# Optimization experiments

Hardware: AMD Instinct MI355X
Metric: run time of the kernel (lower is better)

Reference implementation:

```python
import jax, jax.numpy as jnp
import numpy as np

THRESHOLD = 1.0  # CIF firing threshold (init kwarg)


def setup_inputs() -> dict:
    key = jax.random.key(0)
    k1, k2 = jax.random.split(key)
    B, T, H = 32, 2048, 512
    return {
        "hidden": jax.random.normal(k1, (B, T, H), dtype=jnp.float32),
        "alphas": jax.random.uniform(k2, (B, T), dtype=jnp.float32),
        "integrate": jnp.zeros((B,), dtype=jnp.float32),
        "frame": jnp.zeros((B, H), dtype=jnp.float32),
    }


def cif_scan(hidden, alphas, integrate, frame, threshold):
    """Continuous integrate-and-fire recurrence over time, vectorized over batch.

    hidden: [B,T,H], alphas: [B,T], integrate: [B], frame: [B,H]
    Returns fires [B,T], frames [B,T,H], integrate_new [B], frame_new [B,H].
    """

    def step(carry, inp):
        integ, fr = carry          # [B], [B,H]
        alpha, h_t = inp           # [B], [B,H]
        dist_completion = 1.0 - integ
        integ = integ + alpha
        fire = integ >= threshold                       # [B] bool
        integ_next = jnp.where(fire, integ - 1.0, integ)
        cur = jnp.where(fire, dist_completion, alpha)   # weight spent this step
        rem = alpha - cur                               # leftover weight after firing
        fr_out = fr + cur[:, None] * h_t                # frame recorded at this step
        fr_next = jnp.where(fire[:, None], rem[:, None] * h_t, fr_out)
        return (integ_next, fr_next), (integ, fr_out)

    xs = (jnp.swapaxes(alphas, 0, 1), jnp.swapaxes(hidden, 0, 1))  # time-major
    (integ_f, frame_f), (fires_t, frames_t) = jax.lax.scan(step, (integrate, frame), xs)
    fires = jnp.swapaxes(fires_t, 0, 1)    # [B,T]
    frames = jnp.swapaxes(frames_t, 0, 1)  # [B,T,H]
    return fires, frames, integ_f, frame_f


def reference(hidden, alphas, integrate, frame):
    T = hidden.shape[1]
    fires, frames, integ_new, frame_new = cif_scan(hidden, alphas, integrate, frame, THRESHOLD)
    # torch.index_select(frames[0], 0, nonzero(fires[0] >= threshold)) -> data-dependent
    # shape; emulate with jit-safe padded nonzero (padding rows replicate row 0).
    idx = jnp.nonzero(fires[0] >= THRESHOLD, size=T, fill_value=0)[0]
    frame_sel = frames[0][idx]  # [T, H], first num_fires rows are the fired frames
    return frame_sel, integ_new, frame_new
```

## Files before the change

kernel.cpp:

```cpp
#include <hip/hip_runtime.h>


#define THRESH 1.0f
#define MAX_T 2048

__global__ __launch_bounds__(256) void cif_transpose_kernel(
    const float4* __restrict__ a4, float4* __restrict__ aT4, int B, int T4)
{
    int tid = blockIdx.x * blockDim.x + threadIdx.x;
    if (tid >= B * T4) return;
    int b = tid / T4, c = tid - b * T4;
    aT4[(size_t)c * B + b] = a4[tid];
}

__global__ __launch_bounds__(64) void cif_scan_kernel(
    const float4* __restrict__ aT4,
    const float*  __restrict__ integ0,
    float* __restrict__ gT,
    unsigned long long* __restrict__ fireMask,
    int* __restrict__ rowStart, int* __restrict__ rowEnd, int* __restrict__ rowFlags,
    int* __restrict__ tlast,
    float* __restrict__ integ_out,
    int B, int T)
{
    const int lane = threadIdx.x;
    const int nchunk = T >> 6;
    __shared__ int s_fire[MAX_T];
    __shared__ unsigned long long s_mask[64];
    __shared__ int s_nf, s_f0;

    const bool act = lane < B;
    float integ = act ? integ0[lane] : 0.0f;
    int   lastc = -1;
    unsigned long long lastm = 0;

    float4 bufA[16], bufB[16];

#define LOADCH(buf, c) do { if (act) { \
    _Pragma("unroll") for (int j = 0; j < 16; ++j) \
        buf[j] = aT4[(size_t)((c) * 16 + j) * B + lane]; } } while (0)

#define DOCH(buf, c) do { if (act) { \
    unsigned lo = 0, hi = 0; \
    _Pragma("unroll") for (int j = 0; j < 16; ++j) { \
        const float av[4] = {buf[j].x, buf[j].y, buf[j].z, buf[j].w}; \
        _Pragma("unroll") for (int k = 0; k < 4; ++k) { \
            const int idx = j * 4 + k; \
            const float alpha = av[k]; \
            const float s   = integ + alpha;       \
            const bool fire = (s >= THRESH);       \
            const float sm1 = s - 1.0f;            \
            integ = fire ? sm1 : s; \
            const float gv = fire ? sm1 : alpha;   \
            if (idx < 32) lo |= fire ? (1u << idx) : 0u; \
            else          hi |= fire ? (1u << (idx - 32)) : 0u; \
            gT[(size_t)((c) * 64 + idx) * B + lane] = gv; \
        } } \
    const unsigned long long m = ((unsigned long long)hi << 32) | lo; \
    fireMask[(size_t)(c) * B + lane] = m; \
    if (lane == 0) s_mask[(c)] = m; \
    lastc = m ? (c) : lastc; \
    lastm = m ? m : lastm; \
    } } while (0)

    LOADCH(bufA, 0);
    for (int c = 0; c < nchunk; c += 2) {
        if (c + 1 < nchunk) LOADCH(bufB, c + 1);
        DOCH(bufA, c);
        if (c + 2 < nchunk) LOADCH(bufA, c + 2);
        if (c + 1 < nchunk) DOCH(bufB, c + 1);
    }
#undef LOADCH
#undef DOCH

    if (act) {
        integ_out[lane] = integ;
        tlast[lane] = (lastc >= 0) ? (lastc * 64 + 63 - __clzll(lastm)) : -1;
    }
    __syncthreads();

    unsigned long long m0 = (lane < nchunk) ? s_mask[lane] : 0ull;
    int pc = __popcll(m0);
    int x = pc;
#pragma unroll
    for (int d = 1; d < 64; d <<= 1) {
        int y = __shfl_up(x, d);
        if (lane >= d) x += y;
    }
    const int excl = x - pc;
    if (lane == 63) s_nf = x;
    if (lane == 0)  s_f0 = (int)(m0 & 1ull);
    {
        unsigned long long m = m0; int r = excl;
        while (m) {
            int p = __ffsll((unsigned long long)m) - 1;
            s_fire[r++] = lane * 64 + p;
            m &= m - 1;
        }
    }
    __syncthreads();

    const int nf = s_nf, f0 = s_f0;
    for (int r = lane; r < T; r += 64) {
        int st, en, fl;
        if (r < nf) {
            en = s_fire[r];
            st = (r == 0) ? 0 : s_fire[r - 1];
            fl = ((r == 0) ? 1 : 0) | 2;
        } else {
            st = 0; en = 0; fl = 1 | (f0 ? 2 : 0);
        }
        rowStart[r] = st; rowEnd[r] = en; rowFlags[r] = fl;
    }
}

__global__ __launch_bounds__(128) void cif_out_kernel(
    const float* __restrict__ hidden,
    const float* __restrict__ frame0,
    const float* __restrict__ gT,
    const float* __restrict__ alphas,
    const int* __restrict__ rowStart, const int* __restrict__ rowEnd,
    const int* __restrict__ rowFlags, const int* __restrict__ tlast,
    float* __restrict__ out_sel,
    float* __restrict__ frame_out,
    int B, int T, int H)
{
    const int blk = blockIdx.x;

    if (blk < T) {
        const int r = blk;
        const int start = rowStart[r], end = rowEnd[r], fl = rowFlags[r];
        const float a  = alphas[end];
        const float ge = gT[(size_t)end * B];
        const float wend = (fl & 2) ? (a - ge) : a;
        for (int h0 = threadIdx.x * 4; h0 < H; h0 += 128 * 4) {
            float4 acc = (fl & 1) ? *reinterpret_cast<const float4*>(frame0 + h0)
                                  : make_float4(0.f, 0.f, 0.f, 0.f);
            for (int s = start; s < end; ++s) {
                const float  w  = gT[(size_t)s * B];
                const float4 hv = *reinterpret_cast<const float4*>(hidden + (size_t)s * H + h0);
                acc.x += w * hv.x; acc.y += w * hv.y;
                acc.z += w * hv.z; acc.w += w * hv.w;
            }
            const float4 hv = *reinterpret_cast<const float4*>(hidden + (size_t)end * H + h0);
            acc.x += wend * hv.x; acc.y += wend * hv.y;
            acc.z += wend * hv.z; acc.w += wend * hv.w;
            *reinterpret_cast<float4*>(out_sel + (size_t)r * H + h0) = acc;
        }
    } else {
        const int b  = blk - T;
        const int tl = tlast[b];
        const int start = (tl < 0) ? 0 : tl;
        const float* hb = hidden + (size_t)b * T * H;
        for (int h0 = threadIdx.x * 4; h0 < H; h0 += 128 * 4) {
            float4 acc = (tl < 0) ? *reinterpret_cast<const float4*>(frame0 + (size_t)b * H + h0)
                                  : make_float4(0.f, 0.f, 0.f, 0.f);
            for (int s = start; s < T; ++s) {
                const float  w  = gT[(size_t)s * B + b];
                const float4 hv = *reinterpret_cast<const float4*>(hb + (size_t)s * H + h0);
                acc.x += w * hv.x; acc.y += w * hv.y;
                acc.z += w * hv.z; acc.w += w * hv.w;
            }
            *reinterpret_cast<float4*>(frame_out + (size_t)b * H + h0) = acc;
        }
    }
}

extern "C" void kernel_launch(void* const* d_in, const int* in_sizes, int n_in,
                              void* d_out, int out_size, void* d_ws, size_t ws_size,
                              hipStream_t stream) {
    const float* hidden    = (const float*)d_in[0];
    const float* alphas    = (const float*)d_in[1];
    const float* integrate = (const float*)d_in[2];
    const float* frame     = (const float*)d_in[3];

    const int B = in_sizes[2];
    const int T = in_sizes[1] / B;
    const int H = in_sizes[3] / B;

    float* out       = (float*)d_out;
    float* out_sel   = out;
    float* integ_out = out + (size_t)T * H;
    float* frame_out = integ_out + B;

    char* ws = (char*)d_ws;
    float4* aT4 = (float4*)ws;                 ws += sizeof(float) * (size_t)B * T;
    float*  gT  = (float*)ws;                  ws += sizeof(float) * (size_t)B * T;
    unsigned long long* fireMask = (unsigned long long*)ws; ws += sizeof(unsigned long long) * (size_t)(T / 64) * B;
    int* rowStart = (int*)ws;                  ws += sizeof(int) * T;
    int* rowEnd   = (int*)ws;                  ws += sizeof(int) * T;
    int* rowFlags = (int*)ws;                  ws += sizeof(int) * T;
    int* tlast    = (int*)ws;                  ws += sizeof(int) * B;

    const int T4 = T / 4;
    cif_transpose_kernel<<<(B * T4 + 255) / 256, 256, 0, stream>>>(
        (const float4*)alphas, aT4, B, T4);

    cif_scan_kernel<<<1, 64, 0, stream>>>(
        aT4, integrate, gT, fireMask, rowStart, rowEnd, rowFlags, tlast,
        integ_out, B, T);

    cif_out_kernel<<<T + B, 128, 0, stream>>>(
        hidden, frame, gT, alphas, rowStart, rowEnd, rowFlags, tlast,
        out_sel, frame_out, B, T, H);
}
```

Measured before the change: 239.3 us.

## Split serial CIF scan into fract-only chain pass plus parallel per-chunk replay

The single-wavefront sequential scan is split in two. A lean chain kernel carries the integrator across time using v_fract_f32, storing only the state at each 64-step chunk boundary. A 1024-thread replay kernel then recomputes fires, weights and masks for every (chunk, batch) pair in parallel. This shortens the serial critical path by removing the per-step stores and mask logic. It costs an extra launch and a second read of the alphas, and it assumes fract(integ+alpha) matches the compare-and-subtract-1 update bit for bit.

Result: faster. 206.8 us (-13.6%).

```diff
diff --git a/kernel.cpp b/kernel.cpp
--- a/kernel.cpp
+++ b/kernel.cpp
@@ -2,7 +2,12 @@
 
 
 #define THRESH 1.0f
-#define MAX_T 2048
+#define MAX_T 4096
+#define MAX_CH 64
+
+__device__ __forceinline__ float fract_exact(float x) {
+    float r; asm("v_fract_f32 %0, %1" : "=v"(r) : "v"(x)); return r;
+}
 
 __global__ __launch_bounds__(256) void cif_transpose_kernel(
     const float4* __restrict__ a4, float4* __restrict__ aT4, int B, int T4)
@@ -13,27 +18,17 @@
     aT4[(size_t)c * B + b] = a4[tid];
 }
 
-__global__ __launch_bounds__(64) void cif_scan_kernel(
+__global__ __launch_bounds__(64) void cif_chain_kernel(
     const float4* __restrict__ aT4,
     const float*  __restrict__ integ0,
-    float* __restrict__ gT,
-    unsigned long long* __restrict__ fireMask,
-    int* __restrict__ rowStart, int* __restrict__ rowEnd, int* __restrict__ rowFlags,
-    int* __restrict__ tlast,
+    float* __restrict__ chunkInteg,
     float* __restrict__ integ_out,
     int B, int T)
 {
     const int lane = threadIdx.x;
+    const bool act = lane < B;
     const int nchunk = T >> 6;
-    __shared__ int s_fire[MAX_T];
-    __shared__ unsigned long long s_mask[64];
-    __shared__ int s_nf, s_f0;
-
-    const bool act = lane < B;
     float integ = act ? integ0[lane] : 0.0f;
-    int   lastc = -1;
-    unsigned long long lastm = 0;
-
     float4 bufA[16], bufB[16];
 
 #define LOADCH(buf, c) do { if (act) { \
@@ -41,27 +36,13 @@
         buf[j] = aT4[(size_t)((c) * 16 + j) * B + lane]; } } while (0)
 
 #define DOCH(buf, c) do { if (act) { \
-    unsigned lo = 0, hi = 0; \
+    chunkInteg[(size_t)(c) * B + lane] = integ; \
     _Pragma("unroll") for (int j = 0; j < 16; ++j) { \
-        const float av[4] = {buf[j].x, buf[j].y, buf[j].z, buf[j].w}; \
-        _Pragma("unroll") for (int k = 0; k < 4; ++k) { \
-            const int idx = j * 4 + k; \
-            const float alpha = av[k]; \
-            const float s   = integ + alpha;       \
-            const bool fire = (s >= THRESH);       \
-            const float sm1 = s - 1.0f;            \
-            integ = fire ? sm1 : s; \
-            const float gv = fire ? sm1 : alpha;   \
-            if (idx < 32) lo |= fire ? (1u << idx) : 0u; \
-            else          hi |= fire ? (1u << (idx - 32)) : 0u; \
-            gT[(size_t)((c) * 64 + idx) * B + lane] = gv; \
-        } } \
-    const unsigned long long m = ((unsigned long long)hi << 32) | lo; \
-    fireMask[(size_t)(c) * B + lane] = m; \
-    if (lane == 0) s_mask[(c)] = m; \
-    lastc = m ? (c) : lastc; \
-    lastm = m ? m : lastm; \
-    } } while (0)
+        integ = fract_exact(integ + buf[j].x); \
+        integ = fract_exact(integ + buf[j].y); \
+        integ = fract_exact(integ + buf[j].z); \
+        integ = fract_exact(integ + buf[j].w); \
+    } } } while (0)
 
     LOADCH(bufA, 0);
     for (int c = 0; c < nchunk; c += 2) {
@@ -73,35 +54,81 @@
 #undef LOADCH
 #undef DOCH
 
-    if (act) {
-        integ_out[lane] = integ;
-        tlast[lane] = (lastc >= 0) ? (lastc * 64 + 63 - __clzll(lastm)) : -1;
+    if (act) integ_out[lane] = integ;
+}
+
+__global__ __launch_bounds__(1024) void cif_replay_kernel(
+    const float4* __restrict__ aT4,
+    const float*  __restrict__ chunkInteg,
+    float* __restrict__ gT,
+    int* __restrict__ rowStart, int* __restrict__ rowEnd, int* __restrict__ rowFlags,
+    int* __restrict__ tlast,
+    int B, int T)
+{
+    const int nchunk = T >> 6;
+    const int tid = threadIdx.x;
+    __shared__ unsigned long long s_mask[2048];
+    __shared__ int s_fire[MAX_T];
+    __shared__ int s_nf, s_f0;
+
+    if (tid < nchunk * B) {
+        const int c = tid / B, b = tid - c * B;
+        float integ = chunkInteg[tid];
+        unsigned long long m = 0;
+        for (int j = 0; j < 16; ++j) {
+            const float4 a4 = aT4[(size_t)(c * 16 + j) * B + b];
+            const float av[4] = {a4.x, a4.y, a4.z, a4.w};
+            float gv[4];
+#pragma unroll
+            for (int k = 0; k < 4; ++k) {
+                const int idx = j * 4 + k;
+                const float alpha = av[k];
+                const float s   = integ + alpha;
+                const bool fire = (s >= THRESH);
+                const float sm1 = s - 1.0f;
+                integ = fire ? sm1 : s;
+                gv[k] = fire ? sm1 : alpha;
+                m |= fire ? (1ull << idx) : 0ull;
+            }
+#pragma unroll
+            for (int k = 0; k < 4; ++k)
+                gT[(size_t)(c * 64 + j * 4 + k) * B + b] = gv[k];
+        }
+        s_mask[tid] = m;
     }
     __syncthreads();
 
-    unsigned long long m0 = (lane < nchunk) ? s_mask[lane] : 0ull;
-    int pc = __popcll(m0);
-    int x = pc;
+    if (tid < B) {
+        int tl = -1;
+        for (int c = nchunk - 1; c >= 0; --c) {
+            const unsigned long long mc = s_mask[c * B + tid];
+            if (mc) { tl = c * 64 + 63 - __clzll(mc); break; }
+        }
+        tlast[tid] = tl;
+    }
+
+    if (tid < 64) {
+        unsigned long long m0 = (tid < nchunk) ? s_mask[tid * B] : 0ull;
+        const int pc = __popcll(m0);
+        int x = pc;
 #pragma unroll
-    for (int d = 1; d < 64; d <<= 1) {
-        int y = __shfl_up(x, d);
-        if (lane >= d) x += y;
-    }
-    const int excl = x - pc;
-    if (lane == 63) s_nf = x;
-    if (lane == 0)  s_f0 = (int)(m0 & 1ull);
-    {
-        unsigned long long m = m0; int r = excl;
-        while (m) {
-            int p = __ffsll((unsigned long long)m) - 1;
-            s_fire[r++] = lane * 64 + p;
-            m &= m - 1;
+        for (int d = 1; d < 64; d <<= 1) {
+            const int y = __shfl_up(x, d);
+            if (tid >= d) x += y;
+        }
+        if (tid == 63) s_nf = x;
+        if (tid == 0)  s_f0 = (int)(m0 & 1ull);
+        int r = x - pc;
+        while (m0) {
+            const int p = __ffsll(m0) - 1;
+            s_fire[r++] = tid * 64 + p;
+            m0 &= m0 - 1;
         }
     }
     __syncthreads();
 
     const int nf = s_nf, f0 = s_f0;
-    for (int r = lane; r < T; r += 64) {
+    for (int r = tid; r < T; r += blockDim.x) {
         int st, en, fl;
         if (r < nf) {
             en = s_fire[r];
@@ -184,21 +211,23 @@
     float* frame_out = integ_out + B;
 
     char* ws = (char*)d_ws;
-    float4* aT4 = (float4*)ws;                 ws += sizeof(float) * (size_t)B * T;
-    float*  gT  = (float*)ws;                  ws += sizeof(float) * (size_t)B * T;
-    unsigned long long* fireMask = (unsigned long long*)ws; ws += sizeof(unsigned long long) * (size_t)(T / 64) * B;
-    int* rowStart = (int*)ws;                  ws += sizeof(int) * T;
-    int* rowEnd   = (int*)ws;                  ws += sizeof(int) * T;
-    int* rowFlags = (int*)ws;                  ws += sizeof(int) * T;
-    int* tlast    = (int*)ws;                  ws += sizeof(int) * B;
+    float4* aT4       = (float4*)ws;  ws += sizeof(float) * (size_t)B * T;
+    float*  gT        = (float*)ws;   ws += sizeof(float) * (size_t)B * T;
+    float*  chunkInteg= (float*)ws;   ws += sizeof(float) * (size_t)(T / 64) * B;
+    int* rowStart = (int*)ws;         ws += sizeof(int) * T;
+    int* rowEnd   = (int*)ws;         ws += sizeof(int) * T;
+    int* rowFlags = (int*)ws;         ws += sizeof(int) * T;
+    int* tlast    = (int*)ws;         ws += sizeof(int) * B;
 
     const int T4 = T / 4;
     cif_transpose_kernel<<<(B * T4 + 255) / 256, 256, 0, stream>>>(
         (const float4*)alphas, aT4, B, T4);
 
-    cif_scan_kernel<<<1, 64, 0, stream>>>(
-        aT4, integrate, gT, fireMask, rowStart, rowEnd, rowFlags, tlast,
-        integ_out, B, T);
+    cif_chain_kernel<<<1, 64, 0, stream>>>(
+        aT4, integrate, chunkInteg, integ_out, B, T);
+
+    cif_replay_kernel<<<1, 1024, 0, stream>>>(
+        aT4, chunkInteg, gT, rowStart, rowEnd, rowFlags, tlast, B, T);
 
     cif_out_kernel<<<T + B, 128, 0, stream>>>(
         hidden, frame, gT, alphas, rowStart, rowEnd, rowFlags, tlast,
```
